# Optimization experiments

Hardware: AMD Instinct MI355X
Metric: run time of the kernel (lower is better)

## Reference

```python
import jax, jax.numpy as jnp
import numpy as np

TAU = 2.0        # spikingjelly LIFNode default tau
VTH = 1.0        # v_threshold
ALPHA = 2.0      # ATan surrogate alpha
NUM_HEADS = 8
N_WIN = 8
TOPK = 4


@jax.custom_vjp
def atan_heaviside(x):
    # spike = H(v - v_th), with ATan surrogate gradient
    return (x >= 0.0).astype(x.dtype)

def _ah_fwd(x):
    return atan_heaviside(x), x

def _ah_bwd(x, g):
    half_pi_alpha = np.float32(np.pi / 2.0 * ALPHA)
    return (g * (ALPHA / 2.0) / (1.0 + (half_pi_alpha * x) ** 2),)

atan_heaviside.defvjp(_ah_fwd, _ah_bwd)


def lif(x):
    """Multi-step LIF over leading time dim. decay_input=True, v_reset=0, detach_reset."""
    def step(v, xt):
        v = v + (xt - v) / TAU                      # charge
        s = atan_heaviside(v - VTH)                 # fire
        v = v * (1.0 - jax.lax.stop_gradient(s))    # hard reset (detached)
        return v, s
    _, spikes = jax.lax.scan(step, jnp.zeros_like(x[0]), x)
    return spikes


def setup_inputs() -> dict:
    key = jax.random.key(0)
    k1, k2, k3, k4, k5 = jax.random.split(key, 5)
    T, B, L, C = 4, 4, 1024, 256
    x = jax.random.normal(k1, (T, B, L, C), dtype=jnp.float32)
    w_qkv = jax.random.normal(k2, (C, 3 * C), dtype=jnp.float32) * (C ** -0.5)
    b_qkv = jax.random.normal(k3, (3 * C,), dtype=jnp.float32) * 0.02
    w_proj = jax.random.normal(k4, (C, C), dtype=jnp.float32) * (C ** -0.5)
    b_proj = jax.random.normal(k5, (C,), dtype=jnp.float32) * 0.02
    return {"x": x, "w_qkv": w_qkv, "b_qkv": b_qkv, "w_proj": w_proj, "b_proj": b_proj}


def reference(x, w_qkv, b_qkv, w_proj, b_proj):
    T, B, L, C = x.shape
    hd = C // NUM_HEADS
    win = L // N_WIN
    scale = hd ** -0.5

    # --- region-level routing (on raw input summed over time) ---
    xs = x.sum(axis=0).reshape(B, N_WIN, win, C)
    region = xs.sum(axis=2)                                  # [B, n_win, C]
    attn_r = jnp.einsum('bnc,bmc->bnm', region, region) * (C ** -0.5)
    _, idx = jax.lax.top_k(attn_r, TOPK)                     # [B, n_win, topk] int32

    # --- qkv + LIF spiking ---
    qkv = x @ w_qkv + b_qkv                                  # [T,B,L,3C]
    q, k, v = jnp.split(qkv, 3, axis=-1)
    q, k, v = lif(q), lif(k), lif(v)
    q = q.reshape(T, B, N_WIN, win, NUM_HEADS, hd)
    k = k.reshape(T, B, N_WIN, win, NUM_HEADS, hd)
    v = v.reshape(T, B, N_WIN, win, NUM_HEADS, hd)

    # --- gather routed KV windows (vectorized; topk-major concat like torch.cat) ---
    b_idx = jnp.arange(B)[:, None, None]                     # [B,1,1]
    k_g = k[:, b_idx, idx].reshape(T, B, N_WIN, TOPK * win, NUM_HEADS, hd)
    v_g = v[:, b_idx, idx].reshape(T, B, N_WIN, TOPK * win, NUM_HEADS, hd)

    # --- windowed attention over gathered keys ---
    attn = jnp.einsum('tbnqhd,tbnkhd->tbnhqk', q, k_g) * scale
    attn = jax.nn.softmax(attn, axis=-1)
    out = jnp.einsum('tbnhqk,tbnkhd->tbnqhd', attn, v_g).reshape(T, B, L, C)

    out = lif(out @ w_proj + b_proj)
    return out
```

## Files before the change

kernel.cpp:

```cpp
#include <hip/hip_runtime.h>
#include <cstdint>
#include <cstddef>

#define TT 4
#define BB 4
#define LL 1024
#define CC 256
#define HH 8
#define HD 32
#define NWIN 8
#define WIN 128
#define TOPKN 4
#define C3 768

__global__ __launch_bounds__(256) void region_kernel(const float* __restrict__ x,
                                                     float* __restrict__ region) {
    int bn = blockIdx.x;
    int b = bn >> 3, n = bn & 7;
    int c = threadIdx.x;
    float tot = 0.0f;
    for (int r = 0; r < WIN; ++r) {
        int l = n * WIN + r;
        float s = 0.0f;
        for (int t = 0; t < TT; ++t) {
            s += x[(((size_t)t * BB + b) * LL + l) * CC + c];
        }
        tot += s;
    }
    region[(size_t)bn * CC + c] = tot;
}

__global__ __launch_bounds__(64) void route_kernel(const float* __restrict__ region,
                                                   int* __restrict__ idx) {
    int b = blockIdx.x;
    __shared__ float reg[NWIN][CC];
    __shared__ float attn_r[NWIN][NWIN];
    int tid = threadIdx.x;
    for (int e = tid; e < NWIN * CC; e += 64)
        reg[e >> 8][e & 255] = region[(size_t)b * NWIN * CC + e];
    __syncthreads();
    int n = tid >> 3, m = tid & 7;
    float s = 0.0f;
    for (int c = 0; c < CC; ++c) s += reg[n][c] * reg[m][c];
    attn_r[n][m] = s * 0.0625f;
    __syncthreads();
    if (tid < NWIN) {
        float vals[NWIN];
        for (int m2 = 0; m2 < NWIN; ++m2) vals[m2] = attn_r[tid][m2];
        for (int kk = 0; kk < TOPKN; ++kk) {
            int bi = 0; float bv = vals[0];
            for (int m2 = 1; m2 < NWIN; ++m2) {
                if (vals[m2] > bv) { bv = vals[m2]; bi = m2; }
            }
            idx[(b * NWIN + tid) * TOPKN + kk] = bi;
            vals[bi] = -INFINITY;
        }
    }
}

__global__ __launch_bounds__(256, 3) void gemm_bias128(const float* __restrict__ A,
                                                       const float* __restrict__ W,
                                                       const float* __restrict__ bias,
                                                       float* __restrict__ C,
                                                       int M, int N, int K) {
    const int BM = 128, BN = 128, BK = 16, TM = 8;
    __shared__ float As[BK][BM + 4];
    __shared__ float Bs[BK][136];
    int tid = threadIdx.x;
    int tx = tid & 15, ty = tid >> 4;
    int bm = blockIdx.x * BM, bn = blockIdx.y * BN;
    float acc[TM][8] = {};
    for (int k0 = 0; k0 < K; k0 += BK) {
#pragma unroll
        for (int it = 0; it < 2; ++it) {
            int i = it * 256 + tid;
            int row = i >> 2, kc = (i & 3) * 4;
            float4 v = *(const float4*)(A + (size_t)(bm + row) * K + k0 + kc);
            As[kc + 0][row] = v.x; As[kc + 1][row] = v.y;
            As[kc + 2][row] = v.z; As[kc + 3][row] = v.w;
        }
#pragma unroll
        for (int it = 0; it < 2; ++it) {
            int i = it * 256 + tid;
            int kr = i >> 5, nc = (i & 31) * 4;
            float4 v = *(const float4*)(W + (size_t)(k0 + kr) * N + bn + nc);
            *(float4*)&Bs[kr][nc] = v;
        }
        __syncthreads();
#pragma unroll
        for (int kk = 0; kk < BK; ++kk) {
            float a[TM], bb[8];
            const float4* ap = (const float4*)&As[kk][ty * TM];
            float4 a0 = ap[0], a1 = ap[1];
            a[0]=a0.x; a[1]=a0.y; a[2]=a0.z; a[3]=a0.w;
            a[4]=a1.x; a[5]=a1.y; a[6]=a1.z; a[7]=a1.w;
            float4 b0 = *(const float4*)&Bs[kk][tx * 4];
            float4 b1 = *(const float4*)&Bs[kk][64 + tx * 4];
            bb[0]=b0.x; bb[1]=b0.y; bb[2]=b0.z; bb[3]=b0.w;
            bb[4]=b1.x; bb[5]=b1.y; bb[6]=b1.z; bb[7]=b1.w;
#pragma unroll
            for (int i = 0; i < TM; ++i)
#pragma unroll
                for (int j = 0; j < 8; ++j)
                    acc[i][j] = fmaf(a[i], bb[j], acc[i][j]);
        }
        __syncthreads();
    }
#pragma unroll
    for (int i = 0; i < TM; ++i) {
        int row = bm + ty * TM + i;
        int col0 = bn + tx * 4;
        int col1 = bn + 64 + tx * 4;
        float4 o0 = make_float4(acc[i][0] + bias[col0 + 0], acc[i][1] + bias[col0 + 1],
                                acc[i][2] + bias[col0 + 2], acc[i][3] + bias[col0 + 3]);
        float4 o1 = make_float4(acc[i][4] + bias[col1 + 0], acc[i][5] + bias[col1 + 1],
                                acc[i][6] + bias[col1 + 2], acc[i][7] + bias[col1 + 3]);
        *(float4*)&C[(size_t)row * N + col0] = o0;
        *(float4*)&C[(size_t)row * N + col1] = o1;
    }
}

__global__ __launch_bounds__(256, 4) void gemm_bias64(const float* __restrict__ A,
                                                      const float* __restrict__ W,
                                                      const float* __restrict__ bias,
                                                      float* __restrict__ C,
                                                      int M, int N, int K) {
    const int BM = 64, BN = 64, BK = 16;
    __shared__ float As[BK][BM + 4];
    __shared__ float Bs[BK][72];
    int tid = threadIdx.x;
    int tx = tid & 15, ty = tid >> 4;
    int bm = blockIdx.x * BM, bn = blockIdx.y * BN;
    float acc[4][4] = {};
    for (int k0 = 0; k0 < K; k0 += BK) {
        {
            int row = tid >> 2, kc = (tid & 3) * 4;
            float4 v = *(const float4*)(A + (size_t)(bm + row) * K + k0 + kc);
            As[kc + 0][row] = v.x; As[kc + 1][row] = v.y;
            As[kc + 2][row] = v.z; As[kc + 3][row] = v.w;
        }
        {
            int kr = tid >> 4, nc = (tid & 15) * 4;
            float4 v = *(const float4*)(W + (size_t)(k0 + kr) * N + bn + nc);
            *(float4*)&Bs[kr][nc] = v;
        }
        __syncthreads();
#pragma unroll
        for (int kk = 0; kk < BK; ++kk) {
            float4 av = *(const float4*)&As[kk][ty * 4];
            float4 bv = *(const float4*)&Bs[kk][tx * 4];
            float a[4] = {av.x, av.y, av.z, av.w};
            float bb[4] = {bv.x, bv.y, bv.z, bv.w};
#pragma unroll
            for (int i = 0; i < 4; ++i)
#pragma unroll
                for (int j = 0; j < 4; ++j)
                    acc[i][j] = fmaf(a[i], bb[j], acc[i][j]);
        }
        __syncthreads();
    }
#pragma unroll
    for (int i = 0; i < 4; ++i) {
        int row = bm + ty * 4 + i;
        int col = bn + tx * 4;
        float4 o = make_float4(acc[i][0] + bias[col + 0], acc[i][1] + bias[col + 1],
                               acc[i][2] + bias[col + 2], acc[i][3] + bias[col + 3]);
        *(float4*)&C[(size_t)row * N + col] = o;
    }
}

__global__ __launch_bounds__(256) void lif_kernel(const float* src, float* dst, size_t stride) {
    size_t i = ((size_t)blockIdx.x * blockDim.x + threadIdx.x) * 4;
    float v[4] = {0.f, 0.f, 0.f, 0.f};
    for (int t = 0; t < TT; ++t) {
        float4 xv4 = *(const float4*)(src + (size_t)t * stride + i);
        float xv[4] = {xv4.x, xv4.y, xv4.z, xv4.w};
        float sp[4];
#pragma unroll
        for (int j = 0; j < 4; ++j) {
            v[j] = v[j] + (xv[j] - v[j]) * 0.5f;
            bool fire = (v[j] >= 1.0f);
            sp[j] = fire ? 1.0f : 0.0f;
            v[j] = fire ? 0.0f : v[j];
        }
        *(float4*)(dst + (size_t)t * stride + i) = make_float4(sp[0], sp[1], sp[2], sp[3]);
    }
}

__global__ __launch_bounds__(256) void pack_kernel(const float* __restrict__ spk,
                                                   uint32_t* __restrict__ pk) {
    size_t g = (size_t)blockIdx.x * 256 + threadIdx.x;
    int row = (int)(g >> 9);
    int col = (int)(g & 511);
    float v = spk[(size_t)row * C3 + col];
    unsigned long long m = __ballot(v >= 0.5f);
    int lane = threadIdx.x & 63;
    if ((lane & 31) == 0)
        pk[(size_t)row * 16 + (col >> 5)] = (lane < 32) ? (uint32_t)m : (uint32_t)(m >> 32);
}

__global__ __launch_bounds__(128, 2) void attn_fused(const float* __restrict__ spk,
                                                     const uint32_t* __restrict__ pk,
                                                     const int* __restrict__ idxws,
                                                     float* __restrict__ out) {
    int bid = blockIdx.x;
    int h = bid & 1, hp = (bid >> 1) & 3, n = (bid >> 3) & 7, b = (bid >> 6) & 3, t = bid >> 8;
    __shared__ __align__(16) float Vlds[2][64][32];
    __shared__ float ptab[33][WIN];
    __shared__ __align__(16) uint32_t kbs[4 * WIN];
    int tid = threadIdx.x;
    int qg = tid & 63, dh = tid >> 6;
    int lbase = (t * BB + b) * LL;

    const int* ip = idxws + (b * NWIN + n) * TOPKN;
    int sidx[TOPKN];
    sidx[0] = ip[0]; sidx[1] = ip[1]; sidx[2] = ip[2]; sidx[3] = ip[3];

#pragma unroll 4
    for (int e = tid; e < 512; e += 128) {
        int w = e >> 7;
        int row = sidx[w] * WIN + (e & 127);
        kbs[e] = pk[(size_t)(lbase + row) * 16 + 8 + hp * 2 + h];
    }
    uint32_t qw0 = pk[(size_t)(lbase + n * WIN + qg) * 16 + hp * 2 + h];
    uint32_t qw1 = pk[(size_t)(lbase + n * WIN + qg + 64) * 16 + hp * 2 + h];
    uint32_t qwt = pk[(size_t)(lbase + n * WIN + tid) * 16 + hp * 2 + h];
    __syncthreads();

    const float* vsrc = spk + (size_t)lbase * C3 + 512 + hp * 64 + h * 32
                        + (size_t)(tid >> 3) * C3 + (tid & 7) * 4;
    int wvoff = (tid >> 6) * 1024;

#define STAGE_HALF(hw_)                                                              \
    do {                                                                             \
        int hw = (hw_);                                                              \
        const float* src = vsrc + (size_t)sidx[hw >> 1] * (WIN * C3)                 \
                                + (size_t)(hw & 1) * 64 * C3;                        \
        char* lbasep = (char*)(&Vlds[hw & 1][0][0]) + wvoff;                         \
        _Pragma("unroll")                                                            \
        for (int it = 0; it < 4; ++it) {                                             \
            __builtin_amdgcn_global_load_lds(                                        \
                (const __attribute__((address_space(1))) void*)(src + (size_t)it * 16 * C3), \
                (__attribute__((address_space(3))) void*)(lbasep + it * 2048),       \
                16, 0, 0);                                                           \
        }                                                                            \
    } while (0)

    STAGE_HALF(0);
    STAGE_HALF(1);

    const float ALPHA_SC = 0.17677669529663687f;
    const uint4* kb4 = (const uint4*)kbs;
    int smax = 0;
#pragma unroll 8
    for (int k4 = 0; k4 < 128; ++k4) {
        uint4 w4 = kb4[k4];
        smax = max(smax, __popc(qwt & w4.x));
        smax = max(smax, __popc(qwt & w4.y));
        smax = max(smax, __popc(qwt & w4.z));
        smax = max(smax, __popc(qwt & w4.w));
    }
    float am = __fmul_rn((float)smax, ALPHA_SC);
    float Z = 0.0f;
#pragma unroll 4
    for (int k4 = 0; k4 < 128; ++k4) {
        uint4 w4 = kb4[k4];
        Z += expf(__fsub_rn(__fmul_rn((float)__popc(qwt & w4.x), ALPHA_SC), am));
        Z += expf(__fsub_rn(__fmul_rn((float)__popc(qwt & w4.y), ALPHA_SC), am));
        Z += expf(__fsub_rn(__fmul_rn((float)__popc(qwt & w4.z), ALPHA_SC), am));
        Z += expf(__fsub_rn(__fmul_rn((float)__popc(qwt & w4.w), ALPHA_SC), am));
    }
    for (int s = 0; s <= 32; ++s)
        ptab[s][tid] = expf(__fsub_rn(__fmul_rn((float)s, ALPHA_SC), am)) / Z;

    float acc0[16], acc1[16];
#pragma unroll
    for (int d = 0; d < 16; ++d) { acc0[d] = 0.0f; acc1[d] = 0.0f; }

    asm volatile("s_waitcnt vmcnt(4)" ::: "memory");
    __syncthreads();

#pragma unroll
    for (int hw = 0; hw < 8; ++hw) {
        const uint4* kw4 = kb4 + hw * 16;
        const float* vb = &Vlds[hw & 1][0][dh * 16];
#pragma unroll 2
        for (int g = 0; g < 16; ++g) {
            uint4 kw = kw4[g];
            const float* pr = vb + g * 128;
#pragma unroll
            for (int jp = 0; jp < 2; ++jp) {
                uint32_t ka = (jp == 0) ? kw.x : kw.z;
                uint32_t kb_ = (jp == 0) ? kw.y : kw.w;
                float Pa0 = ptab[__popc(qw0 & ka)][qg];
                float Pa1 = ptab[__popc(qw1 & ka)][qg + 64];
                float Pb0 = ptab[__popc(qw0 & kb_)][qg];
                float Pb1 = ptab[__popc(qw1 & kb_)][qg + 64];
                const float4* va = (const float4*)(pr + jp * 64);
                const float4* vbp = (const float4*)(pr + jp * 64 + 32);
                float4 a0 = va[0], a1 = va[1], a2 = va[2], a3 = va[3];
                float4 b0 = vbp[0], b1 = vbp[1], b2 = vbp[2], b3 = vbp[3];
                acc0[ 0] = fmaf(Pa0, a0.x, acc0[ 0]);  acc1[ 0] = fmaf(Pa1, a0.x, acc1[ 0]);
                acc0[ 1] = fmaf(Pa0, a0.y, acc0[ 1]);  acc1[ 1] = fmaf(Pa1, a0.y, acc1[ 1]);
                acc0[ 2] = fmaf(Pa0, a0.z, acc0[ 2]);  acc1[ 2] = fmaf(Pa1, a0.z, acc1[ 2]);
                acc0[ 3] = fmaf(Pa0, a0.w, acc0[ 3]);  acc1[ 3] = fmaf(Pa1, a0.w, acc1[ 3]);
                acc0[ 4] = fmaf(Pa0, a1.x, acc0[ 4]);  acc1[ 4] = fmaf(Pa1, a1.x, acc1[ 4]);
                acc0[ 5] = fmaf(Pa0, a1.y, acc0[ 5]);  acc1[ 5] = fmaf(Pa1, a1.y, acc1[ 5]);
                acc0[ 6] = fmaf(Pa0, a1.z, acc0[ 6]);  acc1[ 6] = fmaf(Pa1, a1.z, acc1[ 6]);
                acc0[ 7] = fmaf(Pa0, a1.w, acc0[ 7]);  acc1[ 7] = fmaf(Pa1, a1.w, acc1[ 7]);
                acc0[ 8] = fmaf(Pa0, a2.x, acc0[ 8]);  acc1[ 8] = fmaf(Pa1, a2.x, acc1[ 8]);
                acc0[ 9] = fmaf(Pa0, a2.y, acc0[ 9]);  acc1[ 9] = fmaf(Pa1, a2.y, acc1[ 9]);
                acc0[10] = fmaf(Pa0, a2.z, acc0[10]);  acc1[10] = fmaf(Pa1, a2.z, acc1[10]);
                acc0[11] = fmaf(Pa0, a2.w, acc0[11]);  acc1[11] = fmaf(Pa1, a2.w, acc1[11]);
                acc0[12] = fmaf(Pa0, a3.x, acc0[12]);  acc1[12] = fmaf(Pa1, a3.x, acc1[12]);
                acc0[13] = fmaf(Pa0, a3.y, acc0[13]);  acc1[13] = fmaf(Pa1, a3.y, acc1[13]);
                acc0[14] = fmaf(Pa0, a3.z, acc0[14]);  acc1[14] = fmaf(Pa1, a3.z, acc1[14]);
                acc0[15] = fmaf(Pa0, a3.w, acc0[15]);  acc1[15] = fmaf(Pa1, a3.w, acc1[15]);
                acc0[ 0] = fmaf(Pb0, b0.x, acc0[ 0]);  acc1[ 0] = fmaf(Pb1, b0.x, acc1[ 0]);
                acc0[ 1] = fmaf(Pb0, b0.y, acc0[ 1]);  acc1[ 1] = fmaf(Pb1, b0.y, acc1[ 1]);
                acc0[ 2] = fmaf(Pb0, b0.z, acc0[ 2]);  acc1[ 2] = fmaf(Pb1, b0.z, acc1[ 2]);
                acc0[ 3] = fmaf(Pb0, b0.w, acc0[ 3]);  acc1[ 3] = fmaf(Pb1, b0.w, acc1[ 3]);
                acc0[ 4] = fmaf(Pb0, b1.x, acc0[ 4]);  acc1[ 4] = fmaf(Pb1, b1.x, acc1[ 4]);
                acc0[ 5] = fmaf(Pb0, b1.y, acc0[ 5]);  acc1[ 5] = fmaf(Pb1, b1.y, acc1[ 5]);
                acc0[ 6] = fmaf(Pb0, b1.z, acc0[ 6]);  acc1[ 6] = fmaf(Pb1, b1.z, acc1[ 6]);
                acc0[ 7] = fmaf(Pb0, b1.w, acc0[ 7]);  acc1[ 7] = fmaf(Pb1, b1.w, acc1[ 7]);
                acc0[ 8] = fmaf(Pb0, b2.x, acc0[ 8]);  acc1[ 8] = fmaf(Pb1, b2.x, acc1[ 8]);
                acc0[ 9] = fmaf(Pb0, b2.y, acc0[ 9]);  acc1[ 9] = fmaf(Pb1, b2.y, acc1[ 9]);
                acc0[10] = fmaf(Pb0, b2.z, acc0[10]);  acc1[10] = fmaf(Pb1, b2.z, acc1[10]);
                acc0[11] = fmaf(Pb0, b2.w, acc0[11]);  acc1[11] = fmaf(Pb1, b2.w, acc1[11]);
                acc0[12] = fmaf(Pb0, b3.x, acc0[12]);  acc1[12] = fmaf(Pb1, b3.x, acc1[12]);
                acc0[13] = fmaf(Pb0, b3.y, acc0[13]);  acc1[13] = fmaf(Pb1, b3.y, acc1[13]);
                acc0[14] = fmaf(Pb0, b3.z, acc0[14]);  acc1[14] = fmaf(Pb1, b3.z, acc1[14]);
                acc0[15] = fmaf(Pb0, b3.w, acc0[15]);  acc1[15] = fmaf(Pb1, b3.w, acc1[15]);
            }
        }

        if (hw < 7) {
            __syncthreads();
            if (hw < 6) {
                STAGE_HALF(hw + 2);
                asm volatile("s_waitcnt vmcnt(4)" ::: "memory");
            } else {
                asm volatile("s_waitcnt vmcnt(0)" ::: "memory");
            }
            __syncthreads();
        }
    }
#undef STAGE_HALF

    size_t ob0 = (size_t)(lbase + n * WIN + qg) * CC + (hp * 2 + h) * 32 + dh * 16;
    size_t ob1 = ob0 + (size_t)64 * CC;
#pragma unroll
    for (int d = 0; d < 16; ++d) out[ob0 + d] = acc0[d];
#pragma unroll
    for (int d = 0; d < 16; ++d) out[ob1 + d] = acc1[d];
}

extern "C" void kernel_launch(void* const* d_in, const int* in_sizes, int n_in,
                              void* d_out, int out_size, void* d_ws, size_t ws_size,
                              hipStream_t stream) {
    const float* x      = (const float*)d_in[0];
    const float* w_qkv  = (const float*)d_in[1];
    const float* b_qkv  = (const float*)d_in[2];
    const float* w_proj = (const float*)d_in[3];
    const float* b_proj = (const float*)d_in[4];
    float* ws = (float*)d_ws;

    float* qkv      = ws;
    float* attn_out = ws + 12582912;
    float* proj     = ws + 16777216;
    uint32_t* pkb   = (uint32_t*)proj;
    float* region   = ws + 20971520;
    int*   idxp     = (int*)(ws + 20979712);
    float* outp     = (float*)d_out;

    region_kernel<<<dim3(BB * NWIN), dim3(256), 0, stream>>>(x, region);
    route_kernel<<<dim3(BB), dim3(64), 0, stream>>>(region, idxp);
    gemm_bias128<<<dim3(128, 6), dim3(256), 0, stream>>>(x, w_qkv, b_qkv, qkv,
                                                         TT * BB * LL, C3, CC);
    lif_kernel<<<dim3(3072), dim3(256), 0, stream>>>(qkv, qkv, (size_t)BB * LL * C3);
    pack_kernel<<<dim3(32768), dim3(256), 0, stream>>>(qkv, pkb);
    attn_fused<<<dim3(TT * BB * NWIN * 4 * 2), dim3(128), 0, stream>>>(qkv, pkb, idxp, attn_out);
    gemm_bias64<<<dim3(256, 4), dim3(256), 0, stream>>>(attn_out, w_proj, b_proj, proj,
                                                        TT * BB * LL, CC, CC);
    lif_kernel<<<dim3(1024), dim3(256), 0, stream>>>(proj, outp, (size_t)BB * LL * CC);
}
```

Before: 274.5 us.

## Shrink attention V staging to 16-row chunks and split region kernel across channels

```diff
diff --git a/kernel.cpp b/kernel.cpp
--- a/kernel.cpp
+++ b/kernel.cpp
@@ -13,11 +13,11 @@
 #define TOPKN 4
 #define C3 768
 
-__global__ __launch_bounds__(256) void region_kernel(const float* __restrict__ x,
-                                                     float* __restrict__ region) {
+__global__ __launch_bounds__(64) void region_kernel(const float* __restrict__ x,
+                                                    float* __restrict__ region) {
     int bn = blockIdx.x;
     int b = bn >> 3, n = bn & 7;
-    int c = threadIdx.x;
+    int c = blockIdx.y * 64 + threadIdx.x;
     float tot = 0.0f;
     for (int r = 0; r < WIN; ++r) {
         int l = n * WIN + r;
@@ -205,21 +205,22 @@
                                                      float* __restrict__ out) {
     int bid = blockIdx.x;
     int h = bid & 1, hp = (bid >> 1) & 3, n = (bid >> 3) & 7, b = (bid >> 6) & 3, t = bid >> 8;
-    __shared__ __align__(16) float Vlds[2][64][32];
+    __shared__ __align__(16) float Vlds[2][16][32];
     __shared__ float ptab[33][WIN];
     __shared__ __align__(16) uint32_t kbs[4 * WIN];
     int tid = threadIdx.x;
-    int qg = tid & 63, dh = tid >> 6;
+    int qg = tid & 63;
+    int dh = tid >> 6;
     int lbase = (t * BB + b) * LL;
 
     const int* ip = idxws + (b * NWIN + n) * TOPKN;
-    int sidx[TOPKN];
-    sidx[0] = ip[0]; sidx[1] = ip[1]; sidx[2] = ip[2]; sidx[3] = ip[3];
+    int s0r = ip[0], s1r = ip[1], s2r = ip[2], s3r = ip[3];
 
 #pragma unroll 4
     for (int e = tid; e < 512; e += 128) {
         int w = e >> 7;
-        int row = sidx[w] * WIN + (e & 127);
+        int sw = (w == 0) ? s0r : (w == 1) ? s1r : (w == 2) ? s2r : s3r;
+        int row = sw * WIN + (e & 127);
         kbs[e] = pk[(size_t)(lbase + row) * 16 + 8 + hp * 2 + h];
     }
     uint32_t qw0 = pk[(size_t)(lbase + n * WIN + qg) * 16 + hp * 2 + h];
@@ -231,23 +232,21 @@
                         + (size_t)(tid >> 3) * C3 + (tid & 7) * 4;
     int wvoff = (tid >> 6) * 1024;
 
-#define STAGE_HALF(hw_)                                                              \
+#define STAGE_E(hw_)                                                                 \
     do {                                                                             \
         int hw = (hw_);                                                              \
-        const float* src = vsrc + (size_t)sidx[hw >> 1] * (WIN * C3)                 \
-                                + (size_t)(hw & 1) * 64 * C3;                        \
-        char* lbasep = (char*)(&Vlds[hw & 1][0][0]) + wvoff;                         \
-        _Pragma("unroll")                                                            \
-        for (int it = 0; it < 4; ++it) {                                             \
-            __builtin_amdgcn_global_load_lds(                                        \
-                (const __attribute__((address_space(1))) void*)(src + (size_t)it * 16 * C3), \
-                (__attribute__((address_space(3))) void*)(lbasep + it * 2048),       \
-                16, 0, 0);                                                           \
-        }                                                                            \
+        int ww = hw >> 3;                                                            \
+        int sw = (ww == 0) ? s0r : (ww == 1) ? s1r : (ww == 2) ? s2r : s3r;          \
+        const float* src = vsrc + (size_t)sw * (WIN * C3)                            \
+                                + (size_t)(hw & 7) * 16 * C3;                        \
+        char* lb = (char*)(&Vlds[hw & 1][0][0]) + wvoff;                             \
+        __builtin_amdgcn_global_load_lds(                                            \
+            (const __attribute__((address_space(1))) void*)src,                      \
+            (__attribute__((address_space(3))) void*)lb, 16, 0, 0);                  \
     } while (0)
 
-    STAGE_HALF(0);
-    STAGE_HALF(1);
+    STAGE_E(0);
+    STAGE_E(1);
 
     const float ALPHA_SC = 0.17677669529663687f;
     const uint4* kb4 = (const uint4*)kbs;
@@ -277,76 +276,63 @@
 #pragma unroll
     for (int d = 0; d < 16; ++d) { acc0[d] = 0.0f; acc1[d] = 0.0f; }
 
-    asm volatile("s_waitcnt vmcnt(4)" ::: "memory");
+    asm volatile("s_waitcnt vmcnt(1)" ::: "memory");
     __syncthreads();
 
-#pragma unroll
-    for (int hw = 0; hw < 8; ++hw) {
-        const uint4* kw4 = kb4 + hw * 16;
+#pragma unroll 1
+    for (int hw = 0; hw < 32; ++hw) {
+        const uint4* kw4 = kb4 + hw * 4;
         const float* vb = &Vlds[hw & 1][0][dh * 16];
-#pragma unroll 2
-        for (int g = 0; g < 16; ++g) {
+
+        float Pv0[16], Pv1[16];
+#pragma unroll
+        for (int g = 0; g < 4; ++g) {
             uint4 kw = kw4[g];
-            const float* pr = vb + g * 128;
-#pragma unroll
-            for (int jp = 0; jp < 2; ++jp) {
-                uint32_t ka = (jp == 0) ? kw.x : kw.z;
-                uint32_t kb_ = (jp == 0) ? kw.y : kw.w;
-                float Pa0 = ptab[__popc(qw0 & ka)][qg];
-                float Pa1 = ptab[__popc(qw1 & ka)][qg + 64];
-                float Pb0 = ptab[__popc(qw0 & kb_)][qg];
-                float Pb1 = ptab[__popc(qw1 & kb_)][qg + 64];
-                const float4* va = (const float4*)(pr + jp * 64);
-                const float4* vbp = (const float4*)(pr + jp * 64 + 32);
-                float4 a0 = va[0], a1 = va[1], a2 = va[2], a3 = va[3];
-                float4 b0 = vbp[0], b1 = vbp[1], b2 = vbp[2], b3 = vbp[3];
-                acc0[ 0] = fmaf(Pa0, a0.x, acc0[ 0]);  acc1[ 0] = fmaf(Pa1, a0.x, acc1[ 0]);
-                acc0[ 1] = fmaf(Pa0, a0.y, acc0[ 1]);  acc1[ 1] = fmaf(Pa1, a0.y, acc1[ 1]);
-                acc0[ 2] = fmaf(Pa0, a0.z, acc0[ 2]);  acc1[ 2] = fmaf(Pa1, a0.z, acc1[ 2]);
-                acc0[ 3] = fmaf(Pa0, a0.w, acc0[ 3]);  acc1[ 3] = fmaf(Pa1, a0.w, acc1[ 3]);
-                acc0[ 4] = fmaf(Pa0, a1.x, acc0[ 4]);  acc1[ 4] = fmaf(Pa1, a1.x, acc1[ 4]);
-                acc0[ 5] = fmaf(Pa0, a1.y, acc0[ 5]);  acc1[ 5] = fmaf(Pa1, a1.y, acc1[ 5]);
-                acc0[ 6] = fmaf(Pa0, a1.z, acc0[ 6]);  acc1[ 6] = fmaf(Pa1, a1.z, acc1[ 6]);
-                acc0[ 7] = fmaf(Pa0, a1.w, acc0[ 7]);  acc1[ 7] = fmaf(Pa1, a1.w, acc1[ 7]);
-                acc0[ 8] = fmaf(Pa0, a2.x, acc0[ 8]);  acc1[ 8] = fmaf(Pa1, a2.x, acc1[ 8]);
-                acc0[ 9] = fmaf(Pa0, a2.y, acc0[ 9]);  acc1[ 9] = fmaf(Pa1, a2.y, acc1[ 9]);
-                acc0[10] = fmaf(Pa0, a2.z, acc0[10]);  acc1[10] = fmaf(Pa1, a2.z, acc1[10]);
-                acc0[11] = fmaf(Pa0, a2.w, acc0[11]);  acc1[11] = fmaf(Pa1, a2.w, acc1[11]);
-                acc0[12] = fmaf(Pa0, a3.x, acc0[12]);  acc1[12] = fmaf(Pa1, a3.x, acc1[12]);
-                acc0[13] = fmaf(Pa0, a3.y, acc0[13]);  acc1[13] = fmaf(Pa1, a3.y, acc1[13]);
-                acc0[14] = fmaf(Pa0, a3.z, acc0[14]);  acc1[14] = fmaf(Pa1, a3.z, acc1[14]);
-                acc0[15] = fmaf(Pa0, a3.w, acc0[15]);  acc1[15] = fmaf(Pa1, a3.w, acc1[15]);
-                acc0[ 0] = fmaf(Pb0, b0.x, acc0[ 0]);  acc1[ 0] = fmaf(Pb1, b0.x, acc1[ 0]);
-                acc0[ 1] = fmaf(Pb0, b0.y, acc0[ 1]);  acc1[ 1] = fmaf(Pb1, b0.y, acc1[ 1]);
-                acc0[ 2] = fmaf(Pb0, b0.z, acc0[ 2]);  acc1[ 2] = fmaf(Pb1, b0.z, acc1[ 2]);
-                acc0[ 3] = fmaf(Pb0, b0.w, acc0[ 3]);  acc1[ 3] = fmaf(Pb1, b0.w, acc1[ 3]);
-                acc0[ 4] = fmaf(Pb0, b1.x, acc0[ 4]);  acc1[ 4] = fmaf(Pb1, b1.x, acc1[ 4]);
-                acc0[ 5] = fmaf(Pb0, b1.y, acc0[ 5]);  acc1[ 5] = fmaf(Pb1, b1.y, acc1[ 5]);
-                acc0[ 6] = fmaf(Pb0, b1.z, acc0[ 6]);  acc1[ 6] = fmaf(Pb1, b1.z, acc1[ 6]);
-                acc0[ 7] = fmaf(Pb0, b1.w, acc0[ 7]);  acc1[ 7] = fmaf(Pb1, b1.w, acc1[ 7]);
-                acc0[ 8] = fmaf(Pb0, b2.x, acc0[ 8]);  acc1[ 8] = fmaf(Pb1, b2.x, acc1[ 8]);
-                acc0[ 9] = fmaf(Pb0, b2.y, acc0[ 9]);  acc1[ 9] = fmaf(Pb1, b2.y, acc1[ 9]);
-                acc0[10] = fmaf(Pb0, b2.z, acc0[10]);  acc1[10] = fmaf(Pb1, b2.z, acc1[10]);
-                acc0[11] = fmaf(Pb0, b2.w, acc0[11]);  acc1[11] = fmaf(Pb1, b2.w, acc1[11]);
-                acc0[12] = fmaf(Pb0, b3.x, acc0[12]);  acc1[12] = fmaf(Pb1, b3.x, acc1[12]);
-                acc0[13] = fmaf(Pb0, b3.y, acc0[13]);  acc1[13] = fmaf(Pb1, b3.y, acc1[13]);
-                acc0[14] = fmaf(Pb0, b3.z, acc0[14]);  acc1[14] = fmaf(Pb1, b3.z, acc1[14]);
-                acc0[15] = fmaf(Pb0, b3.w, acc0[15]);  acc1[15] = fmaf(Pb1, b3.w, acc1[15]);
-            }
-        }
-
-        if (hw < 7) {
+            Pv0[g*4+0] = ptab[__popc(qw0 & kw.x)][qg];
+            Pv1[g*4+0] = ptab[__popc(qw1 & kw.x)][qg + 64];
+            Pv0[g*4+1] = ptab[__popc(qw0 & kw.y)][qg];
+            Pv1[g*4+1] = ptab[__popc(qw1 & kw.y)][qg + 64];
+            Pv0[g*4+2] = ptab[__popc(qw0 & kw.z)][qg];
+            Pv1[g*4+2] = ptab[__popc(qw1 & kw.z)][qg + 64];
+            Pv0[g*4+3] = ptab[__popc(qw0 & kw.w)][qg];
+            Pv1[g*4+3] = ptab[__popc(qw1 & kw.w)][qg + 64];
+        }
+
+#pragma unroll
+        for (int r = 0; r < 16; ++r) {
+            const float4* vp = (const float4*)(vb + r * 32);
+            float4 v0 = vp[0], v1 = vp[1], v2 = vp[2], v3 = vp[3];
+            float P0 = Pv0[r], P1 = Pv1[r];
+            acc0[ 0] = fmaf(P0, v0.x, acc0[ 0]);  acc1[ 0] = fmaf(P1, v0.x, acc1[ 0]);
+            acc0[ 1] = fmaf(P0, v0.y, acc0[ 1]);  acc1[ 1] = fmaf(P1, v0.y, acc1[ 1]);
+            acc0[ 2] = fmaf(P0, v0.z, acc0[ 2]);  acc1[ 2] = fmaf(P1, v0.z, acc1[ 2]);
+            acc0[ 3] = fmaf(P0, v0.w, acc0[ 3]);  acc1[ 3] = fmaf(P1, v0.w, acc1[ 3]);
+            acc0[ 4] = fmaf(P0, v1.x, acc0[ 4]);  acc1[ 4] = fmaf(P1, v1.x, acc1[ 4]);
+            acc0[ 5] = fmaf(P0, v1.y, acc0[ 5]);  acc1[ 5] = fmaf(P1, v1.y, acc1[ 5]);
+            acc0[ 6] = fmaf(P0, v1.z, acc0[ 6]);  acc1[ 6] = fmaf(P1, v1.z, acc1[ 6]);
+            acc0[ 7] = fmaf(P0, v1.w, acc0[ 7]);  acc1[ 7] = fmaf(P1, v1.w, acc1[ 7]);
+            acc0[ 8] = fmaf(P0, v2.x, acc0[ 8]);  acc1[ 8] = fmaf(P1, v2.x, acc1[ 8]);
+            acc0[ 9] = fmaf(P0, v2.y, acc0[ 9]);  acc1[ 9] = fmaf(P1, v2.y, acc1[ 9]);
+            acc0[10] = fmaf(P0, v2.z, acc0[10]);  acc1[10] = fmaf(P1, v2.z, acc1[10]);
+            acc0[11] = fmaf(P0, v2.w, acc0[11]);  acc1[11] = fmaf(P1, v2.w, acc1[11]);
+            acc0[12] = fmaf(P0, v3.x, acc0[12]);  acc1[12] = fmaf(P1, v3.x, acc1[12]);
+            acc0[13] = fmaf(P0, v3.y, acc0[13]);  acc1[13] = fmaf(P1, v3.y, acc1[13]);
+            acc0[14] = fmaf(P0, v3.z, acc0[14]);  acc1[14] = fmaf(P1, v3.z, acc1[14]);
+            acc0[15] = fmaf(P0, v3.w, acc0[15]);  acc1[15] = fmaf(P1, v3.w, acc1[15]);
+        }
+
+        if (hw < 31) {
             __syncthreads();
-            if (hw < 6) {
-                STAGE_HALF(hw + 2);
-                asm volatile("s_waitcnt vmcnt(4)" ::: "memory");
+            if (hw < 30) {
+                STAGE_E(hw + 2);
+                asm volatile("s_waitcnt vmcnt(1)" ::: "memory");
             } else {
                 asm volatile("s_waitcnt vmcnt(0)" ::: "memory");
             }
             __syncthreads();
         }
     }
-#undef STAGE_HALF
+#undef STAGE_E
 
     size_t ob0 = (size_t)(lbase + n * WIN + qg) * CC + (hp * 2 + h) * 32 + dh * 16;
     size_t ob1 = ob0 + (size_t)64 * CC;
@@ -374,7 +360,7 @@
     int*   idxp     = (int*)(ws + 20979712);
     float* outp     = (float*)d_out;
 
-    region_kernel<<<dim3(BB * NWIN), dim3(256), 0, stream>>>(x, region);
+    region_kernel<<<dim3(BB * NWIN, 4), dim3(64), 0, stream>>>(x, region);
     route_kernel<<<dim3(BB), dim3(64), 0, stream>>>(region, idxp);
     gemm_bias128<<<dim3(128, 6), dim3(256), 0, stream>>>(x, w_qkv, b_qkv, qkv,
                                                          TT * BB * LL, C3, CC);
```

Result: slower. 576.2 us (+109.9%).

## Use one query row per thread in attention and split region reduction across channels

Applied to the files above, without the earlier changes.

```diff
diff --git a/kernel.cpp b/kernel.cpp
--- a/kernel.cpp
+++ b/kernel.cpp
@@ -13,11 +13,11 @@
 #define TOPKN 4
 #define C3 768
 
-__global__ __launch_bounds__(256) void region_kernel(const float* __restrict__ x,
-                                                     float* __restrict__ region) {
+__global__ __launch_bounds__(64) void region_kernel(const float* __restrict__ x,
+                                                    float* __restrict__ region) {
     int bn = blockIdx.x;
     int b = bn >> 3, n = bn & 7;
-    int c = threadIdx.x;
+    int c = blockIdx.y * 64 + threadIdx.x;
     float tot = 0.0f;
     for (int r = 0; r < WIN; ++r) {
         int l = n * WIN + r;
@@ -199,7 +199,7 @@
         pk[(size_t)row * 16 + (col >> 5)] = (lane < 32) ? (uint32_t)m : (uint32_t)(m >> 32);
 }
 
-__global__ __launch_bounds__(128, 2) void attn_fused(const float* __restrict__ spk,
+__global__ __launch_bounds__(256, 4) void attn_fused(const float* __restrict__ spk,
                                                      const uint32_t* __restrict__ pk,
                                                      const int* __restrict__ idxws,
                                                      float* __restrict__ out) {
@@ -209,22 +209,20 @@
     __shared__ float ptab[33][WIN];
     __shared__ __align__(16) uint32_t kbs[4 * WIN];
     int tid = threadIdx.x;
-    int qg = tid & 63, dh = tid >> 6;
+    int q = tid & 127, dh = tid >> 7;
     int lbase = (t * BB + b) * LL;
 
     const int* ip = idxws + (b * NWIN + n) * TOPKN;
-    int sidx[TOPKN];
-    sidx[0] = ip[0]; sidx[1] = ip[1]; sidx[2] = ip[2]; sidx[3] = ip[3];
-
-#pragma unroll 4
-    for (int e = tid; e < 512; e += 128) {
+    int s0r = ip[0], s1r = ip[1], s2r = ip[2], s3r = ip[3];
+
+#pragma unroll 2
+    for (int e = tid; e < 512; e += 256) {
         int w = e >> 7;
-        int row = sidx[w] * WIN + (e & 127);
+        int sw = (w == 0) ? s0r : (w == 1) ? s1r : (w == 2) ? s2r : s3r;
+        int row = sw * WIN + (e & 127);
         kbs[e] = pk[(size_t)(lbase + row) * 16 + 8 + hp * 2 + h];
     }
-    uint32_t qw0 = pk[(size_t)(lbase + n * WIN + qg) * 16 + hp * 2 + h];
-    uint32_t qw1 = pk[(size_t)(lbase + n * WIN + qg + 64) * 16 + hp * 2 + h];
-    uint32_t qwt = pk[(size_t)(lbase + n * WIN + tid) * 16 + hp * 2 + h];
+    uint32_t qw = pk[(size_t)(lbase + n * WIN + q) * 16 + hp * 2 + h];
     __syncthreads();
 
     const float* vsrc = spk + (size_t)lbase * C3 + 512 + hp * 64 + h * 32
@@ -234,16 +232,17 @@
 #define STAGE_HALF(hw_)                                                              \
     do {                                                                             \
         int hw = (hw_);                                                              \
-        const float* src = vsrc + (size_t)sidx[hw >> 1] * (WIN * C3)                 \
+        int ww = hw >> 1;                                                            \
+        int sw = (ww == 0) ? s0r : (ww == 1) ? s1r : (ww == 2) ? s2r : s3r;          \
+        const float* src = vsrc + (size_t)sw * (WIN * C3)                            \
                                 + (size_t)(hw & 1) * 64 * C3;                        \
-        char* lbasep = (char*)(&Vlds[hw & 1][0][0]) + wvoff;                         \
-        _Pragma("unroll")                                                            \
-        for (int it = 0; it < 4; ++it) {                                             \
-            __builtin_amdgcn_global_load_lds(                                        \
-                (const __attribute__((address_space(1))) void*)(src + (size_t)it * 16 * C3), \
-                (__attribute__((address_space(3))) void*)(lbasep + it * 2048),       \
-                16, 0, 0);                                                           \
-        }                                                                            \
+        char* lb = (char*)(&Vlds[hw & 1][0][0]) + wvoff;                             \
+        __builtin_amdgcn_global_load_lds(                                            \
+            (const __attribute__((address_space(1))) void*)src,                      \
+            (__attribute__((address_space(3))) void*)lb, 16, 0, 0);                  \
+        __builtin_amdgcn_global_load_lds(                                            \
+            (const __attribute__((address_space(1))) void*)(src + 32 * C3),          \
+            (__attribute__((address_space(3))) void*)(lb + 4096), 16, 0, 0);         \
     } while (0)
 
     STAGE_HALF(0);
@@ -251,33 +250,35 @@
 
     const float ALPHA_SC = 0.17677669529663687f;
     const uint4* kb4 = (const uint4*)kbs;
-    int smax = 0;
+    if (tid < 128) {
+        int smax = 0;
 #pragma unroll 8
-    for (int k4 = 0; k4 < 128; ++k4) {
-        uint4 w4 = kb4[k4];
-        smax = max(smax, __popc(qwt & w4.x));
-        smax = max(smax, __popc(qwt & w4.y));
-        smax = max(smax, __popc(qwt & w4.z));
-        smax = max(smax, __popc(qwt & w4.w));
-    }
-    float am = __fmul_rn((float)smax, ALPHA_SC);
-    float Z = 0.0f;
+        for (int k4 = 0; k4 < 128; ++k4) {
+            uint4 w4 = kb4[k4];
+            smax = max(smax, __popc(qw & w4.x));
+            smax = max(smax, __popc(qw & w4.y));
+            smax = max(smax, __popc(qw & w4.z));
+            smax = max(smax, __popc(qw & w4.w));
+        }
+        float am = __fmul_rn((float)smax, ALPHA_SC);
+        float Z = 0.0f;
 #pragma unroll 4
-    for (int k4 = 0; k4 < 128; ++k4) {
-        uint4 w4 = kb4[k4];
-        Z += expf(__fsub_rn(__fmul_rn((float)__popc(qwt & w4.x), ALPHA_SC), am));
-        Z += expf(__fsub_rn(__fmul_rn((float)__popc(qwt & w4.y), ALPHA_SC), am));
-        Z += expf(__fsub_rn(__fmul_rn((float)__popc(qwt & w4.z), ALPHA_SC), am));
-        Z += expf(__fsub_rn(__fmul_rn((float)__popc(qwt & w4.w), ALPHA_SC), am));
-    }
-    for (int s = 0; s <= 32; ++s)
-        ptab[s][tid] = expf(__fsub_rn(__fmul_rn((float)s, ALPHA_SC), am)) / Z;
-
-    float acc0[16], acc1[16];
-#pragma unroll
-    for (int d = 0; d < 16; ++d) { acc0[d] = 0.0f; acc1[d] = 0.0f; }
-
-    asm volatile("s_waitcnt vmcnt(4)" ::: "memory");
+        for (int k4 = 0; k4 < 128; ++k4) {
+            uint4 w4 = kb4[k4];
+            Z += expf(__fsub_rn(__fmul_rn((float)__popc(qw & w4.x), ALPHA_SC), am));
+            Z += expf(__fsub_rn(__fmul_rn((float)__popc(qw & w4.y), ALPHA_SC), am));
+            Z += expf(__fsub_rn(__fmul_rn((float)__popc(qw & w4.z), ALPHA_SC), am));
+            Z += expf(__fsub_rn(__fmul_rn((float)__popc(qw & w4.w), ALPHA_SC), am));
+        }
+        for (int s = 0; s <= 32; ++s)
+            ptab[s][tid] = expf(__fsub_rn(__fmul_rn((float)s, ALPHA_SC), am)) / Z;
+    }
+
+    float acc[16];
+#pragma unroll
+    for (int d = 0; d < 16; ++d) acc[d] = 0.0f;
+
+    asm volatile("s_waitcnt vmcnt(2)" ::: "memory");
     __syncthreads();
 
 #pragma unroll
@@ -292,46 +293,44 @@
             for (int jp = 0; jp < 2; ++jp) {
                 uint32_t ka = (jp == 0) ? kw.x : kw.z;
                 uint32_t kb_ = (jp == 0) ? kw.y : kw.w;
-                float Pa0 = ptab[__popc(qw0 & ka)][qg];
-                float Pa1 = ptab[__popc(qw1 & ka)][qg + 64];
-                float Pb0 = ptab[__popc(qw0 & kb_)][qg];
-                float Pb1 = ptab[__popc(qw1 & kb_)][qg + 64];
+                float Pa = ptab[__popc(qw & ka)][q];
+                float Pb = ptab[__popc(qw & kb_)][q];
                 const float4* va = (const float4*)(pr + jp * 64);
                 const float4* vbp = (const float4*)(pr + jp * 64 + 32);
                 float4 a0 = va[0], a1 = va[1], a2 = va[2], a3 = va[3];
                 float4 b0 = vbp[0], b1 = vbp[1], b2 = vbp[2], b3 = vbp[3];
-                acc0[ 0] = fmaf(Pa0, a0.x, acc0[ 0]);  acc1[ 0] = fmaf(Pa1, a0.x, acc1[ 0]);
-                acc0[ 1] = fmaf(Pa0, a0.y, acc0[ 1]);  acc1[ 1] = fmaf(Pa1, a0.y, acc1[ 1]);
-                acc0[ 2] = fmaf(Pa0, a0.z, acc0[ 2]);  acc1[ 2] = fmaf(Pa1, a0.z, acc1[ 2]);
-                acc0[ 3] = fmaf(Pa0, a0.w, acc0[ 3]);  acc1[ 3] = fmaf(Pa1, a0.w, acc1[ 3]);
-                acc0[ 4] = fmaf(Pa0, a1.x, acc0[ 4]);  acc1[ 4] = fmaf(Pa1, a1.x, acc1[ 4]);
-                acc0[ 5] = fmaf(Pa0, a1.y, acc0[ 5]);  acc1[ 5] = fmaf(Pa1, a1.y, acc1[ 5]);
-                acc0[ 6] = fmaf(Pa0, a1.z, acc0[ 6]);  acc1[ 6] = fmaf(Pa1, a1.z, acc1[ 6]);
-                acc0[ 7] = fmaf(Pa0, a1.w, acc0[ 7]);  acc1[ 7] = fmaf(Pa1, a1.w, acc1[ 7]);
-                acc0[ 8] = fmaf(Pa0, a2.x, acc0[ 8]);  acc1[ 8] = fmaf(Pa1, a2.x, acc1[ 8]);
-                acc0[ 9] = fmaf(Pa0, a2.y, acc0[ 9]);  acc1[ 9] = fmaf(Pa1, a2.y, acc1[ 9]);
-                acc0[10] = fmaf(Pa0, a2.z, acc0[10]);  acc1[10] = fmaf(Pa1, a2.z, acc1[10]);
-                acc0[11] = fmaf(Pa0, a2.w, acc0[11]);  acc1[11] = fmaf(Pa1, a2.w, acc1[11]);
-                acc0[12] = fmaf(Pa0, a3.x, acc0[12]);  acc1[12] = fmaf(Pa1, a3.x, acc1[12]);
-                acc0[13] = fmaf(Pa0, a3.y, acc0[13]);  acc1[13] = fmaf(Pa1, a3.y, acc1[13]);
-                acc0[14] = fmaf(Pa0, a3.z, acc0[14]);  acc1[14] = fmaf(Pa1, a3.z, acc1[14]);
-                acc0[15] = fmaf(Pa0, a3.w, acc0[15]);  acc1[15] = fmaf(Pa1, a3.w, acc1[15]);
-                acc0[ 0] = fmaf(Pb0, b0.x, acc0[ 0]);  acc1[ 0] = fmaf(Pb1, b0.x, acc1[ 0]);
-                acc0[ 1] = fmaf(Pb0, b0.y, acc0[ 1]);  acc1[ 1] = fmaf(Pb1, b0.y, acc1[ 1]);
-                acc0[ 2] = fmaf(Pb0, b0.z, acc0[ 2]);  acc1[ 2] = fmaf(Pb1, b0.z, acc1[ 2]);
-                acc0[ 3] = fmaf(Pb0, b0.w, acc0[ 3]);  acc1[ 3] = fmaf(Pb1, b0.w, acc1[ 3]);
-                acc0[ 4] = fmaf(Pb0, b1.x, acc0[ 4]);  acc1[ 4] = fmaf(Pb1, b1.x, acc1[ 4]);
-                acc0[ 5] = fmaf(Pb0, b1.y, acc0[ 5]);  acc1[ 5] = fmaf(Pb1, b1.y, acc1[ 5]);
-                acc0[ 6] = fmaf(Pb0, b1.z, acc0[ 6]);  acc1[ 6] = fmaf(Pb1, b1.z, acc1[ 6]);
-                acc0[ 7] = fmaf(Pb0, b1.w, acc0[ 7]);  acc1[ 7] = fmaf(Pb1, b1.w, acc1[ 7]);
-                acc0[ 8] = fmaf(Pb0, b2.x, acc0[ 8]);  acc1[ 8] = fmaf(Pb1, b2.x, acc1[ 8]);
-                acc0[ 9] = fmaf(Pb0, b2.y, acc0[ 9]);  acc1[ 9] = fmaf(Pb1, b2.y, acc1[ 9]);
-                acc0[10] = fmaf(Pb0, b2.z, acc0[10]);  acc1[10] = fmaf(Pb1, b2.z, acc1[10]);
-                acc0[11] = fmaf(Pb0, b2.w, acc0[11]);  acc1[11] = fmaf(Pb1, b2.w, acc1[11]);
-                acc0[12] = fmaf(Pb0, b3.x, acc0[12]);  acc1[12] = fmaf(Pb1, b3.x, acc1[12]);
-                acc0[13] = fmaf(Pb0, b3.y, acc0[13]);  acc1[13] = fmaf(Pb1, b3.y, acc1[13]);
-                acc0[14] = fmaf(Pb0, b3.z, acc0[14]);  acc1[14] = fmaf(Pb1, b3.z, acc1[14]);
-                acc0[15] = fmaf(Pb0, b3.w, acc0[15]);  acc1[15] = fmaf(Pb1, b3.w, acc1[15]);
+                acc[ 0] = fmaf(Pa, a0.x, acc[ 0]);
+                acc[ 1] = fmaf(Pa, a0.y, acc[ 1]);
+                acc[ 2] = fmaf(Pa, a0.z, acc[ 2]);
+                acc[ 3] = fmaf(Pa, a0.w, acc[ 3]);
+                acc[ 4] = fmaf(Pa, a1.x, acc[ 4]);
+                acc[ 5] = fmaf(Pa, a1.y, acc[ 5]);
+                acc[ 6] = fmaf(Pa, a1.z, acc[ 6]);
+                acc[ 7] = fmaf(Pa, a1.w, acc[ 7]);
+                acc[ 8] = fmaf(Pa, a2.x, acc[ 8]);
+                acc[ 9] = fmaf(Pa, a2.y, acc[ 9]);
+                acc[10] = fmaf(Pa, a2.z, acc[10]);
+                acc[11] = fmaf(Pa, a2.w, acc[11]);
+                acc[12] = fmaf(Pa, a3.x, acc[12]);
+                acc[13] = fmaf(Pa, a3.y, acc[13]);
+                acc[14] = fmaf(Pa, a3.z, acc[14]);
+                acc[15] = fmaf(Pa, a3.w, acc[15]);
+                acc[ 0] = fmaf(Pb, b0.x, acc[ 0]);
+                acc[ 1] = fmaf(Pb, b0.y, acc[ 1]);
+                acc[ 2] = fmaf(Pb, b0.z, acc[ 2]);
+                acc[ 3] = fmaf(Pb, b0.w, acc[ 3]);
+                acc[ 4] = fmaf(Pb, b1.x, acc[ 4]);
+                acc[ 5] = fmaf(Pb, b1.y, acc[ 5]);
+                acc[ 6] = fmaf(Pb, b1.z, acc[ 6]);
+                acc[ 7] = fmaf(Pb, b1.w, acc[ 7]);
+                acc[ 8] = fmaf(Pb, b2.x, acc[ 8]);
+                acc[ 9] = fmaf(Pb, b2.y, acc[ 9]);
+                acc[10] = fmaf(Pb, b2.z, acc[10]);
+                acc[11] = fmaf(Pb, b2.w, acc[11]);
+                acc[12] = fmaf(Pb, b3.x, acc[12]);
+                acc[13] = fmaf(Pb, b3.y, acc[13]);
+                acc[14] = fmaf(Pb, b3.z, acc[14]);
+                acc[15] = fmaf(Pb, b3.w, acc[15]);
             }
         }
 
@@ -339,7 +338,7 @@
             __syncthreads();
             if (hw < 6) {
                 STAGE_HALF(hw + 2);
-                asm volatile("s_waitcnt vmcnt(4)" ::: "memory");
+                asm volatile("s_waitcnt vmcnt(2)" ::: "memory");
             } else {
                 asm volatile("s_waitcnt vmcnt(0)" ::: "memory");
             }
@@ -348,12 +347,9 @@
     }
 #undef STAGE_HALF
 
-    size_t ob0 = (size_t)(lbase + n * WIN + qg) * CC + (hp * 2 + h) * 32 + dh * 16;
-    size_t ob1 = ob0 + (size_t)64 * CC;
-#pragma unroll
-    for (int d = 0; d < 16; ++d) out[ob0 + d] = acc0[d];
-#pragma unroll
-    for (int d = 0; d < 16; ++d) out[ob1 + d] = acc1[d];
+    size_t ob = (size_t)(lbase + n * WIN + q) * CC + (hp * 2 + h) * 32 + dh * 16;
+#pragma unroll
+    for (int d = 0; d < 16; ++d) out[ob + d] = acc[d];
 }
 
 extern "C" void kernel_launch(void* const* d_in, const int* in_sizes, int n_in,
@@ -374,13 +370,13 @@
     int*   idxp     = (int*)(ws + 20979712);
     float* outp     = (float*)d_out;
 
-    region_kernel<<<dim3(BB * NWIN), dim3(256), 0, stream>>>(x, region);
+    region_kernel<<<dim3(BB * NWIN, 4), dim3(64), 0, stream>>>(x, region);
     route_kernel<<<dim3(BB), dim3(64), 0, stream>>>(region, idxp);
     gemm_bias128<<<dim3(128, 6), dim3(256), 0, stream>>>(x, w_qkv, b_qkv, qkv,
                                                          TT * BB * LL, C3, CC);
     lif_kernel<<<dim3(3072), dim3(256), 0, stream>>>(qkv, qkv, (size_t)BB * LL * C3);
     pack_kernel<<<dim3(32768), dim3(256), 0, stream>>>(qkv, pkb);
-    attn_fused<<<dim3(TT * BB * NWIN * 4 * 2), dim3(128), 0, stream>>>(qkv, pkb, idxp, attn_out);
+    attn_fused<<<dim3(TT * BB * NWIN * 4 * 2), dim3(256), 0, stream>>>(qkv, pkb, idxp, attn_out);
     gemm_bias64<<<dim3(256, 4), dim3(256), 0, stream>>>(attn_out, w_proj, b_proj, proj,
                                                         TT * BB * LL, CC, CC);
     lif_kernel<<<dim3(1024), dim3(256), 0, stream>>>(proj, outp, (size_t)BB * LL * CC);
```

Result: slower. 280.9 us (+2.3%).
